# Kernel tuning notes

Measured on AMD Instinct MI355X. Metric: run time of the kernel, lower is better.

## Reference

```python
import jax, jax.numpy as jnp
import numpy as np

N_NODES = 100000
N_EDGES = 1600000
N_FEAT = 128
HID = 64


def setup_inputs() -> dict:
    key = jax.random.key(0)
    ks = jax.random.split(key, 8)
    s = 0.05
    return {
        "x": jax.random.normal(ks[0], (N_NODES, N_FEAT), jnp.float32),
        "edge_index": jax.random.randint(ks[1], (2, N_EDGES), 0, N_NODES, jnp.int64),
        "labels": jax.random.randint(ks[2], (N_NODES, 1), 0, 2, jnp.int32),
        "W1": jax.random.normal(ks[3], (N_FEAT, HID), jnp.float32) * s,
        "b1": jnp.zeros((HID,), jnp.float32),
        "W2": jax.random.normal(ks[4], (HID, HID), jnp.float32) * s,
        "b2": jnp.zeros((HID,), jnp.float32),
        "W3": jax.random.normal(ks[5], (HID, HID), jnp.float32) * s,
        "b3": jnp.zeros((HID,), jnp.float32),
        "lW1": jax.random.normal(ks[6], (HID, 8), jnp.float32) * s,
        "lb1": jnp.zeros((8,), jnp.float32),
        "lW2": jax.random.normal(ks[7], (8, 1), jnp.float32) * s,
        "lb2": jnp.zeros((1,), jnp.float32),
    }


def reference(x, edge_index, labels, W1, b1, W2, b2, W3, b3, lW1, lb1, lW2, lb2):
    n = x.shape[0]
    # PyG GCNConv: add self-loops, symmetric D^{-1/2}(A+I)D^{-1/2} normalization
    loop = jnp.arange(n)
    row = jnp.concatenate([edge_index[0], loop])  # sources
    col = jnp.concatenate([edge_index[1], loop])  # targets (aggregation)
    deg = jax.ops.segment_sum(jnp.ones(col.shape, x.dtype), col, num_segments=n)
    dinv = jax.lax.rsqrt(deg)  # deg >= 1 thanks to self loops
    norm = dinv[row] * dinv[col]  # [E+N]

    def gcn(h, W, b):
        m = (h @ W)[row] * norm[:, None]  # gather + scale per edge
        return jax.ops.segment_sum(m, col, num_segments=n) + b

    h = jax.nn.relu(gcn(x, W1, b1))   # dropout inactive in eval mode
    h = jax.nn.relu(gcn(h, W2, b2))
    h = jax.nn.relu(gcn(h, W3, b3))
    h = jax.nn.relu(h @ lW1 + lb1)
    p = jax.nn.sigmoid(h @ lW2 + lb2)  # [N,1]

    y = labels.astype(x.dtype)
    # generate_weights(labels): class-balance weights (minority class up-weighted)
    pm = jnp.mean(y)
    w = y * (1.0 - pm) + (1.0 - y) * pm
    eps = 1e-7
    pc = jnp.clip(p, eps, 1.0 - eps)
    bce = -(y * jnp.log(pc) + (1.0 - y) * jnp.log(1.0 - pc))
    loss = jnp.mean(w * bce)
    return loss, p
```

## Files before the change

### kernel.cpp

```cpp
#include <hip/hip_runtime.h>
#include <cstdint>
#include <cstddef>

typedef __attribute__((ext_vector_type(8))) short short8;
typedef __attribute__((ext_vector_type(4))) float f32x4;
typedef __attribute__((ext_vector_type(2))) float f32x2;

#define NBLK 512
#define NBLK_SHIFT 9

__device__ inline unsigned short f2bf(float f) {
  union { float f; unsigned int u; } x; x.f = f;
  unsigned int r = x.u + 0x7FFFu + ((x.u >> 16) & 1u);
  return (unsigned short)(r >> 16);
}
__device__ inline float bf2f(unsigned short s) {
  union { unsigned int u; float f; } x; x.u = ((unsigned int)s) << 16;
  return x.f;
}


__global__ __launch_bounds__(256) void hist_kernel(const int* __restrict__ cols,
                                                   int* __restrict__ histG,
                                                   const int* __restrict__ labels,
                                                   float* __restrict__ pmsum,
                                                   const float* __restrict__ W1,
                                                   const float* __restrict__ W2,
                                                   const float* __restrict__ W3,
                                                   unsigned short* __restrict__ Wt1,
                                                   unsigned short* __restrict__ Wt2,
                                                   unsigned short* __restrict__ Wt3,
                                                   int E, int N, int NBUCK) {
  __shared__ int h[512];
  if (blockIdx.x < 3) {
    const float* W; unsigned short* Wt; int K;
    if (blockIdx.x == 0)      { W = W1; Wt = Wt1; K = 128; }
    else if (blockIdx.x == 1) { W = W2; Wt = Wt2; K = 64; }
    else                      { W = W3; Wt = Wt3; K = 64; }
    int total = K * 64;
    for (int i = threadIdx.x; i < total; i += 256) {
      int n = i / K, k = i - n * K;
      Wt[i] = f2bf(W[k * 64 + n]);
    }
  }
  {
    int chunkL = (N + NBLK - 1) / NBLK;
    int ls = blockIdx.x * chunkL;
    int le = min(N, ls + chunkL);
    float v = 0.f;
    for (int i = ls + threadIdx.x; i < le; i += 256) v += (float)labels[i];
#pragma unroll
    for (int o = 32; o > 0; o >>= 1) v += __shfl_down(v, o);
    __shared__ float sl[4];
    if ((threadIdx.x & 63) == 0) sl[threadIdx.x >> 6] = v;
    __syncthreads();
    if (threadIdx.x == 0) {
      float t = sl[0] + sl[1] + sl[2] + sl[3];
      if (t != 0.f) atomicAdd(pmsum, t);
    }
  }
  for (int i = threadIdx.x; i < NBUCK; i += 256) h[i] = 0;
  __syncthreads();
  int chunk = (E + NBLK - 1) / NBLK;
  int s = blockIdx.x * chunk;
  int e = min(E, s + chunk);
  for (int i = s + threadIdx.x; i < e; i += 256) atomicAdd(&h[cols[i] >> 8], 1);
  __syncthreads();
  for (int i = threadIdx.x; i < NBUCK; i += 256)
    histG[blockIdx.x * NBUCK + i] = h[i];
}


__global__ __launch_bounds__(256) void scan_partials_t(const int* __restrict__ histG,
                                                       int* __restrict__ partials,
                                                       int total, int NBUCK) {
  int i = blockIdx.x * 256 + threadIdx.x;
  int v = 0;
  if (i < total) {
    int bucket = i >> NBLK_SHIFT, blk = i & (NBLK - 1);
    v = histG[blk * NBUCK + bucket];
  }
#pragma unroll
  for (int o = 32; o > 0; o >>= 1) v += __shfl_down(v, o);
  __shared__ int s[4];
  if ((threadIdx.x & 63) == 0) s[threadIdx.x >> 6] = v;
  __syncthreads();
  if (threadIdx.x == 0) partials[blockIdx.x] = s[0] + s[1] + s[2] + s[3];
}

__global__ __launch_bounds__(256) void scan_block(int* __restrict__ partials, int nb,
                                                  float* __restrict__ loss) {
  __shared__ int tmp[256];
  __shared__ int carry;
  int tid = threadIdx.x;
  if (tid == 0) { carry = 0; *loss = 0.f; }
  __syncthreads();
  for (int base = 0; base < nb; base += 256) {
    int i = base + tid;
    int v = (i < nb) ? partials[i] : 0;
    tmp[tid] = v;
    __syncthreads();
    int incl = v;
    for (int o = 1; o < 256; o <<= 1) {
      int t = (tid >= o) ? tmp[tid - o] : 0;
      __syncthreads();
      incl += t;
      tmp[tid] = incl;
      __syncthreads();
    }
    int total = tmp[255];
    int c = carry;
    if (i < nb) partials[i] = c + incl - v;
    __syncthreads();
    if (tid == 0) carry = c + total;
    __syncthreads();
  }
}

__global__ __launch_bounds__(256) void scan_final_t(const int* __restrict__ histG,
                                                    const int* __restrict__ partials,
                                                    int* __restrict__ scannedG,
                                                    int total, int NBUCK) {
  __shared__ int tmp[256];
  int tid = threadIdx.x;
  int i = blockIdx.x * 256 + tid;
  int bucket = i >> NBLK_SHIFT, blk = i & (NBLK - 1);
  int v = (i < total) ? histG[blk * NBUCK + bucket] : 0;
  tmp[tid] = v;
  __syncthreads();
  int incl = v;
  for (int o = 1; o < 256; o <<= 1) {
    int t = (tid >= o) ? tmp[tid - o] : 0;
    __syncthreads();
    incl += t;
    tmp[tid] = incl;
    __syncthreads();
  }
  if (i < total) scannedG[blk * NBUCK + bucket] = partials[blockIdx.x] + incl - v;
}


__global__ __launch_bounds__(256) void scatter_kernel(const int* __restrict__ rows,
                                                      const int* __restrict__ cols,
                                                      const int* __restrict__ scannedG,
                                                      unsigned int* __restrict__ packed,
                                                      int E, int NBUCK) {
  __shared__ int cur[512];
  for (int i = threadIdx.x; i < NBUCK; i += 256)
    cur[i] = scannedG[blockIdx.x * NBUCK + i];
  __syncthreads();
  int chunk = (E + NBLK - 1) / NBLK;
  int s = blockIdx.x * chunk;
  int e = min(E, s + chunk);
  for (int i = s + threadIdx.x; i < e; i += 256) {
    int c = cols[i];
    int r = rows[i];
    int pos = atomicAdd(&cur[c >> 8], 1);
    packed[pos] = ((unsigned int)(c & 255) << 24) | (unsigned int)r;
  }
}


__global__ __launch_bounds__(1024) void csr_finalize(const unsigned int* __restrict__ packed,
                                                     const int* __restrict__ scannedG,
                                                     int* __restrict__ sorted_src,
                                                     int* __restrict__ offsets,
                                                     float* __restrict__ dinv,
                                                     int N, int E, int NBUCK) {
  __shared__ int h[256];
  __shared__ int tmp[256];
  __shared__ int cur[256];
  int b = blockIdx.x;
  int tid = threadIdx.x;
  int base = scannedG[b];
  int end = (b + 1 < NBUCK) ? scannedG[b + 1] : E;
  if (tid < 256) h[tid] = 0;
  __syncthreads();
  for (int i = base + tid; i < end; i += 1024)
    atomicAdd(&h[packed[i] >> 24], 1);
  __syncthreads();
  if (tid < 256) {
    int v = h[tid];
    tmp[tid] = v;
  }
  __syncthreads();
  if (tid < 256) {
    int v = h[tid];
    int incl = v;
    for (int o = 1; o < 256; o <<= 1) {
      int t = (tid >= o) ? tmp[tid - o] : 0;
      __syncthreads();
      incl += t;
      tmp[tid] = incl;
      __syncthreads();
    }
    int excl = incl - v;
    int node = b * 256 + tid;
    if (node < N) {
      offsets[node] = base + excl;
      dinv[node] = rsqrtf((float)(v + 1));
    }
    cur[tid] = base + excl;
    if (b == NBUCK - 1 && tid == 0) offsets[N] = E;
  } else {
    for (int o = 1; o < 256; o <<= 1) { __syncthreads(); __syncthreads(); }
  }
  __syncthreads();
  for (int i = base + tid; i < end; i += 1024) {
    unsigned int p = packed[i];
    int pos = atomicAdd(&cur[p >> 24], 1);
    sorted_src[pos] = (int)(p & 0xFFFFFFu);
  }
}


template <int K, bool F32IN>
__global__ __launch_bounds__(256) void mfma_gemm(const void* __restrict__ hv,
                                                 const unsigned short* __restrict__ Wt,
                                                 const float* __restrict__ dinv,
                                                 unsigned char* __restrict__ out, int N) {
  __shared__ unsigned short tile[4][16 * 68];
  int w = threadIdx.x >> 6, lane = threadIdx.x & 63;
  int m = lane & 15, quad = lane >> 4;
  int m0 = blockIdx.x * 64 + w * 16;
  int rowA = m0 + m;
  bool rowOK = rowA < N;
  f32x4 acc[4] = {{0.f,0.f,0.f,0.f},{0.f,0.f,0.f,0.f},{0.f,0.f,0.f,0.f},{0.f,0.f,0.f,0.f}};
#pragma unroll
  for (int kc = 0; kc < K / 32; ++kc) {
    short8 a = {0, 0, 0, 0, 0, 0, 0, 0};
    if (rowOK) {
      if (F32IN) {
        const float* hp = (const float*)hv + (size_t)rowA * K + kc * 32 + quad * 8;
        float4 p0 = ((const float4*)hp)[0];
        float4 p1 = ((const float4*)hp)[1];
        a[0] = (short)f2bf(p0.x); a[1] = (short)f2bf(p0.y);
        a[2] = (short)f2bf(p0.z); a[3] = (short)f2bf(p0.w);
        a[4] = (short)f2bf(p1.x); a[5] = (short)f2bf(p1.y);
        a[6] = (short)f2bf(p1.z); a[7] = (short)f2bf(p1.w);
      } else {
        a = *(const short8*)((const unsigned short*)hv + (size_t)rowA * K + kc * 32 + quad * 8);
      }
    }
#pragma unroll
    for (int t = 0; t < 4; ++t) {
      short8 b = *(const short8*)(Wt + (size_t)(t * 16 + m) * K + kc * 32 + quad * 8);
      acc[t] = __builtin_amdgcn_mfma_f32_16x16x32_bf16(a, b, acc[t], 0, 0, 0);
    }
  }
  unsigned short* tw = tile[w];
#pragma unroll
  for (int r = 0; r < 4; ++r) {
    int row = quad * 4 + r;
    int gr = m0 + row;
    float dv = dinv[gr < N ? gr : 0];
#pragma unroll
    for (int t = 0; t < 4; ++t)
      tw[row * 68 + t * 16 + m] = f2bf(acc[t][r] * dv);
  }
#pragma unroll
  for (int p = 0; p < 4; ++p) {
    int row = p * 4 + (lane >> 4);
    int ch = lane & 15;
    int gr = m0 + row;
    if (gr < N) {
      uint2 v = *(const uint2*)(tw + row * 68 + ch * 4);
      float f0 = bf2f((unsigned short)(v.x & 0xFFFFu));
      float f1 = bf2f((unsigned short)(v.x >> 16));
      float f2 = bf2f((unsigned short)(v.y & 0xFFFFu));
      float f3 = bf2f((unsigned short)(v.y >> 16));
      int pk = 0;
      pk = __builtin_amdgcn_cvt_pk_fp8_f32(f0, f1, pk, false);
      pk = __builtin_amdgcn_cvt_pk_fp8_f32(f2, f3, pk, true);
      *(unsigned int*)(out + (size_t)gr * 64 + ch * 4) = (unsigned int)pk;
    }
  }
}


__global__ __launch_bounds__(256) void aggregate(const unsigned char* __restrict__ A8,
                                                 const int* __restrict__ offsets,
                                                 const int* __restrict__ sorted_src,
                                                 const float* __restrict__ dinv,
                                                 const float* __restrict__ bias,
                                                 unsigned short* __restrict__ out, int N) {
  int c = blockIdx.x * 16 + (threadIdx.x >> 4);
  if (c >= N) return;
  int l = threadIdx.x & 15;
  int qbase = threadIdx.x & 48;
  int g = l >> 3;
  int fi = l & 7;
  int s = offsets[c], e = offsets[c + 1];
  float dc = dinv[c];
  uint2 svr = *(const uint2*)(A8 + (size_t)c * 64 + fi * 8);
  f32x2 a0 = {0.f, 0.f}, a1 = {0.f, 0.f}, a2 = {0.f, 0.f}, a3 = {0.f, 0.f};
  for (int base = s; base < e; base += 16) {
    int idx = base + l;
    int r = (idx < e) ? sorted_src[idx] : 0;
    int cnt = e - base; if (cnt > 16) cnt = 16;
    int rj[8];
#pragma unroll
    for (int t = 0; t < 8; ++t) rj[t] = __shfl(r, qbase + t * 2 + g);
#pragma unroll
    for (int t = 0; t < 8; ++t) {
      if (t * 2 + g < cnt) {
        uint2 v = *(const uint2*)(A8 + ((size_t)(unsigned int)rj[t] << 6) + fi * 8);
        a0 += __builtin_amdgcn_cvt_pk_f32_fp8((int)v.x, false);
        a1 += __builtin_amdgcn_cvt_pk_f32_fp8((int)v.x, true);
        a2 += __builtin_amdgcn_cvt_pk_f32_fp8((int)v.y, false);
        a3 += __builtin_amdgcn_cvt_pk_f32_fp8((int)v.y, true);
      }
    }
  }
  float acc[8] = {a0[0], a0[1], a1[0], a1[1], a2[0], a2[1], a3[0], a3[1]};
#pragma unroll
  for (int q = 0; q < 8; ++q)
    acc[q] += __shfl_xor(acc[q], 8);
  if (g == 0) {
    f32x2 s0 = __builtin_amdgcn_cvt_pk_f32_fp8((int)svr.x, false);
    f32x2 s1 = __builtin_amdgcn_cvt_pk_f32_fp8((int)svr.x, true);
    f32x2 s2 = __builtin_amdgcn_cvt_pk_f32_fp8((int)svr.y, false);
    f32x2 s3 = __builtin_amdgcn_cvt_pk_f32_fp8((int)svr.y, true);
    float sf[8] = {s0[0], s0[1], s1[0], s1[1], s2[0], s2[1], s3[0], s3[1]};
    short8 ov;
#pragma unroll
    for (int q = 0; q < 8; ++q) {
      float v = fmaf(acc[q] + sf[q], dc, bias[fi * 8 + q]);
      ov[q] = (short)f2bf(v > 0.f ? v : 0.f);
    }
    *(short8*)(out + (size_t)c * 64 + fi * 8) = ov;
  }
}


__global__ __launch_bounds__(256) void head_loss_kernel(const unsigned short* __restrict__ h,
                                                        const float* __restrict__ lW1,
                                                        const float* __restrict__ lb1,
                                                        const float* __restrict__ lW2,
                                                        const float* __restrict__ lb2,
                                                        const int* __restrict__ labels,
                                                        const float* __restrict__ pmsum,
                                                        float* __restrict__ p,
                                                        float* __restrict__ loss, int N) {
  int n = blockIdx.x * 256 + threadIdx.x;
  float contrib = 0.f;
  if (n < N) {
    float acc[8];
#pragma unroll
    for (int j = 0; j < 8; ++j) acc[j] = lb1[j];
    const unsigned short* hr = h + (size_t)n * 64;
#pragma unroll
    for (int ch = 0; ch < 8; ++ch) {
      short8 hv8 = ((const short8*)hr)[ch];
#pragma unroll
      for (int q = 0; q < 8; ++q) {
        float v = bf2f((unsigned short)hv8[q]);
        int k = ch * 8 + q;
#pragma unroll
        for (int j = 0; j < 8; ++j) acc[j] = fmaf(v, lW1[k * 8 + j], acc[j]);
      }
    }
    float s = lb2[0];
#pragma unroll
    for (int j = 0; j < 8; ++j) {
      float a = acc[j] > 0.f ? acc[j] : 0.f;
      s = fmaf(a, lW2[j], s);
    }
    float pv = 1.0f / (1.0f + expf(-s));
    p[n] = pv;
    float pm = *pmsum / (float)N;
    float y = (float)labels[n];
    float w = y * (1.f - pm) + (1.f - y) * pm;
    float pc = fminf(fmaxf(pv, 1e-7f), 1.f - 1e-7f);
    float bce = -(y * logf(pc) + (1.f - y) * logf(1.f - pc));
    contrib = w * bce / (float)N;
  }
#pragma unroll
  for (int o = 32; o > 0; o >>= 1) contrib += __shfl_down(contrib, o);
  __shared__ float sh[4];
  int lane = threadIdx.x & 63, w = threadIdx.x >> 6;
  if (lane == 0) sh[w] = contrib;
  __syncthreads();
  if (threadIdx.x == 0) atomicAdd(loss, sh[0] + sh[1] + sh[2] + sh[3]);
}


extern "C" void kernel_launch(void* const* d_in, const int* in_sizes, int n_in,
                              void* d_out, int out_size, void* d_ws, size_t ws_size,
                              hipStream_t stream) {
  const float* x      = (const float*)d_in[0];
  const int*   ei     = (const int*)d_in[1];
  const int*   labels = (const int*)d_in[2];
  const float* W1 = (const float*)d_in[3];
  const float* b1 = (const float*)d_in[4];
  const float* W2 = (const float*)d_in[5];
  const float* b2 = (const float*)d_in[6];
  const float* W3 = (const float*)d_in[7];
  const float* b3 = (const float*)d_in[8];
  const float* lW1 = (const float*)d_in[9];
  const float* lb1 = (const float*)d_in[10];
  const float* lW2 = (const float*)d_in[11];
  const float* lb2 = (const float*)d_in[12];

  int N = in_sizes[2];
  int E = in_sizes[1] / 2;
  const int* rows = ei;
  const int* cols = ei + E;

  int nb = (N + 255) / 256;
  int Npad = (N + 63) & ~63;
  int NBUCK = (N + 255) >> 8;
  int totalH = NBUCK * NBLK;
  int nb2 = (totalH + 255) / 256;

  char* ws = (char*)d_ws;
  unsigned char*  A8  = (unsigned char*)ws;
  unsigned short* H   = (unsigned short*)(ws + (size_t)Npad * 64);
  unsigned short* Wt1 = H + (size_t)Npad * 64;
  unsigned short* Wt2 = Wt1 + 64 * 128;
  unsigned short* Wt3 = Wt2 + 64 * 64;
  float* dinv     = (float*)(Wt3 + 64 * 64);
  int*   offsets  = (int*)(dinv + N);
  int*   histG    = offsets + N + 1;
  int*   scanned  = histG + totalH;
  unsigned int* packed = (unsigned int*)(scanned + totalH);
  int*   sorted   = (int*)(packed + E);
  int*   partials = sorted + E;
  float* pmsum    = (float*)(partials + nb2);

  float* loss = (float*)d_out;
  float* p    = (float*)d_out + 1;

  int gemmBlocks = Npad / 64;
  int aggBlocks  = (N + 15) / 16;

  hipMemsetAsync(pmsum, 0, sizeof(float), stream);
  hist_kernel<<<NBLK, 256, 0, stream>>>(cols, histG, labels, pmsum,
                                        W1, W2, W3, Wt1, Wt2, Wt3, E, N, NBUCK);
  scan_partials_t<<<nb2, 256, 0, stream>>>(histG, partials, totalH, NBUCK);
  scan_block<<<1, 256, 0, stream>>>(partials, nb2, loss);
  scan_final_t<<<nb2, 256, 0, stream>>>(histG, partials, scanned, totalH, NBUCK);
  scatter_kernel<<<NBLK, 256, 0, stream>>>(rows, cols, scanned, packed, E, NBUCK);
  csr_finalize<<<NBUCK, 1024, 0, stream>>>(packed, scanned, sorted, offsets, dinv, N, E, NBUCK);

  mfma_gemm<128, true><<<gemmBlocks, 256, 0, stream>>>(x, Wt1, dinv, A8, N);
  aggregate<<<aggBlocks, 256, 0, stream>>>(A8, offsets, sorted, dinv, b1, H, N);

  mfma_gemm<64, false><<<gemmBlocks, 256, 0, stream>>>(H, Wt2, dinv, A8, N);
  aggregate<<<aggBlocks, 256, 0, stream>>>(A8, offsets, sorted, dinv, b2, H, N);

  mfma_gemm<64, false><<<gemmBlocks, 256, 0, stream>>>(H, Wt3, dinv, A8, N);
  aggregate<<<aggBlocks, 256, 0, stream>>>(A8, offsets, sorted, dinv, b3, H, N);

  head_loss_kernel<<<nb, 256, 0, stream>>>(H, lW1, lb1, lW2, lb2, labels, pmsum, p, loss, N);
}
```

Baseline: 305.2 us.

## Split feature matrices into two 32-column planes and aggregate each plane separately

The GEMM output (fp8) and hidden activations (bf16) are stored as two planes of 32 features each instead of interleaved 64-wide rows. Aggregation runs twice per layer, once per plane, so each pass gathers from a smaller working set (32 bytes per node, about 3.2 MB) that fits better in cache. Each 16-lane group now handles 4 edges in parallel instead of 2. The change also adds nontemporal loads of edge indices and nontemporal output stores. In exchange the edge list and offsets are read twice per layer and there are extra launches.

```diff
diff --git a/kernel.cpp b/kernel.cpp
--- a/kernel.cpp
+++ b/kernel.cpp
@@ -218,7 +218,8 @@
 __global__ __launch_bounds__(256) void mfma_gemm(const void* __restrict__ hv,
                                                  const unsigned short* __restrict__ Wt,
                                                  const float* __restrict__ dinv,
-                                                 unsigned char* __restrict__ out, int N) {
+                                                 unsigned char* __restrict__ out,
+                                                 int N, int Npad) {
   __shared__ unsigned short tile[4][16 * 68];
   int w = threadIdx.x >> 6, lane = threadIdx.x & 63;
   int m = lane & 15, quad = lane >> 4;
@@ -239,7 +240,9 @@
         a[4] = (short)f2bf(p1.x); a[5] = (short)f2bf(p1.y);
         a[6] = (short)f2bf(p1.z); a[7] = (short)f2bf(p1.w);
       } else {
-        a = *(const short8*)((const unsigned short*)hv + (size_t)rowA * K + kc * 32 + quad * 8);
+        const unsigned short* hp = (const unsigned short*)hv +
+            (size_t)kc * ((size_t)Npad * 32) + (size_t)rowA * 32 + quad * 8;
+        a = *(const short8*)hp;
       }
     }
 #pragma unroll
@@ -258,6 +261,7 @@
     for (int t = 0; t < 4; ++t)
       tw[row * 68 + t * 16 + m] = f2bf(acc[t][r] * dv);
   }
+  size_t planeB = (size_t)Npad * 32;
 #pragma unroll
   for (int p = 0; p < 4; ++p) {
     int row = p * 4 + (lane >> 4);
@@ -272,39 +276,42 @@
       int pk = 0;
       pk = __builtin_amdgcn_cvt_pk_fp8_f32(f0, f1, pk, false);
       pk = __builtin_amdgcn_cvt_pk_fp8_f32(f2, f3, pk, true);
-      *(unsigned int*)(out + (size_t)gr * 64 + ch * 4) = (unsigned int)pk;
-    }
-  }
-}
-
-
-__global__ __launch_bounds__(256) void aggregate(const unsigned char* __restrict__ A8,
-                                                 const int* __restrict__ offsets,
-                                                 const int* __restrict__ sorted_src,
-                                                 const float* __restrict__ dinv,
-                                                 const float* __restrict__ bias,
-                                                 unsigned short* __restrict__ out, int N) {
+      *(unsigned int*)(out + (size_t)(ch >> 3) * planeB +
+                       ((size_t)gr << 5) + (size_t)(ch & 7) * 4) = (unsigned int)pk;
+    }
+  }
+}
+
+
+__global__ __launch_bounds__(256) void aggregate_plane(const unsigned char* __restrict__ A8,
+                                                       const int* __restrict__ offsets,
+                                                       const int* __restrict__ sorted_src,
+                                                       const float* __restrict__ dinv,
+                                                       const float* __restrict__ bias,
+                                                       unsigned short* __restrict__ out,
+                                                       int N, int Npad, int plane) {
   int c = blockIdx.x * 16 + (threadIdx.x >> 4);
   if (c >= N) return;
   int l = threadIdx.x & 15;
   int qbase = threadIdx.x & 48;
-  int g = l >> 3;
-  int fi = l & 7;
+  int g = l >> 2;
+  int fi = l & 3;
+  const unsigned char* P = A8 + (size_t)plane * ((size_t)Npad * 32);
   int s = offsets[c], e = offsets[c + 1];
   float dc = dinv[c];
-  uint2 svr = *(const uint2*)(A8 + (size_t)c * 64 + fi * 8);
+  uint2 svr = *(const uint2*)(P + ((size_t)c << 5) + fi * 8);
   f32x2 a0 = {0.f, 0.f}, a1 = {0.f, 0.f}, a2 = {0.f, 0.f}, a3 = {0.f, 0.f};
   for (int base = s; base < e; base += 16) {
     int idx = base + l;
-    int r = (idx < e) ? sorted_src[idx] : 0;
+    int r = (idx < e) ? __builtin_nontemporal_load(sorted_src + idx) : 0;
     int cnt = e - base; if (cnt > 16) cnt = 16;
-    int rj[8];
-#pragma unroll
-    for (int t = 0; t < 8; ++t) rj[t] = __shfl(r, qbase + t * 2 + g);
-#pragma unroll
-    for (int t = 0; t < 8; ++t) {
-      if (t * 2 + g < cnt) {
-        uint2 v = *(const uint2*)(A8 + ((size_t)(unsigned int)rj[t] << 6) + fi * 8);
+    int rj[4];
+#pragma unroll
+    for (int t = 0; t < 4; ++t) rj[t] = __shfl(r, qbase + t * 4 + g);
+#pragma unroll
+    for (int t = 0; t < 4; ++t) {
+      if (t * 4 + g < cnt) {
+        uint2 v = *(const uint2*)(P + ((size_t)(unsigned int)rj[t] << 5) + fi * 8);
         a0 += __builtin_amdgcn_cvt_pk_f32_fp8((int)v.x, false);
         a1 += __builtin_amdgcn_cvt_pk_f32_fp8((int)v.x, true);
         a2 += __builtin_amdgcn_cvt_pk_f32_fp8((int)v.y, false);
@@ -314,21 +321,25 @@
   }
   float acc[8] = {a0[0], a0[1], a1[0], a1[1], a2[0], a2[1], a3[0], a3[1]};
 #pragma unroll
-  for (int q = 0; q < 8; ++q)
+  for (int q = 0; q < 8; ++q) {
+    acc[q] += __shfl_xor(acc[q], 4);
     acc[q] += __shfl_xor(acc[q], 8);
+  }
   if (g == 0) {
     f32x2 s0 = __builtin_amdgcn_cvt_pk_f32_fp8((int)svr.x, false);
     f32x2 s1 = __builtin_amdgcn_cvt_pk_f32_fp8((int)svr.x, true);
     f32x2 s2 = __builtin_amdgcn_cvt_pk_f32_fp8((int)svr.y, false);
     f32x2 s3 = __builtin_amdgcn_cvt_pk_f32_fp8((int)svr.y, true);
     float sf[8] = {s0[0], s0[1], s1[0], s1[1], s2[0], s2[1], s3[0], s3[1]};
+    const float* bp = bias + plane * 32 + fi * 8;
     short8 ov;
 #pragma unroll
     for (int q = 0; q < 8; ++q) {
-      float v = fmaf(acc[q] + sf[q], dc, bias[fi * 8 + q]);
+      float v = fmaf(acc[q] + sf[q], dc, bp[q]);
       ov[q] = (short)f2bf(v > 0.f ? v : 0.f);
     }
-    *(short8*)(out + (size_t)c * 64 + fi * 8) = ov;
+    __builtin_nontemporal_store(ov,
+        (short8*)(out + (size_t)plane * ((size_t)Npad * 32) + (size_t)c * 32 + fi * 8));
   }
 }
 
@@ -341,17 +352,19 @@
                                                         const int* __restrict__ labels,
                                                         const float* __restrict__ pmsum,
                                                         float* __restrict__ p,
-                                                        float* __restrict__ loss, int N) {
+                                                        float* __restrict__ loss,
+                                                        int N, int Npad) {
   int n = blockIdx.x * 256 + threadIdx.x;
   float contrib = 0.f;
   if (n < N) {
     float acc[8];
 #pragma unroll
     for (int j = 0; j < 8; ++j) acc[j] = lb1[j];
-    const unsigned short* hr = h + (size_t)n * 64;
+    size_t planeS = (size_t)Npad * 32;
+    const unsigned short* hr = h + (size_t)n * 32;
 #pragma unroll
     for (int ch = 0; ch < 8; ++ch) {
-      short8 hv8 = ((const short8*)hr)[ch];
+      short8 hv8 = *(const short8*)(hr + (size_t)(ch >> 2) * planeS + (ch & 3) * 8);
 #pragma unroll
       for (int q = 0; q < 8; ++q) {
         float v = bf2f((unsigned short)hv8[q]);
@@ -443,14 +456,17 @@
   scatter_kernel<<<NBLK, 256, 0, stream>>>(rows, cols, scanned, packed, E, NBUCK);
   csr_finalize<<<NBUCK, 1024, 0, stream>>>(packed, scanned, sorted, offsets, dinv, N, E, NBUCK);
 
-  mfma_gemm<128, true><<<gemmBlocks, 256, 0, stream>>>(x, Wt1, dinv, A8, N);
-  aggregate<<<aggBlocks, 256, 0, stream>>>(A8, offsets, sorted, dinv, b1, H, N);
-
-  mfma_gemm<64, false><<<gemmBlocks, 256, 0, stream>>>(H, Wt2, dinv, A8, N);
-  aggregate<<<aggBlocks, 256, 0, stream>>>(A8, offsets, sorted, dinv, b2, H, N);
-
-  mfma_gemm<64, false><<<gemmBlocks, 256, 0, stream>>>(H, Wt3, dinv, A8, N);
-  aggregate<<<aggBlocks, 256, 0, stream>>>(A8, offsets, sorted, dinv, b3, H, N);
-
-  head_loss_kernel<<<nb, 256, 0, stream>>>(H, lW1, lb1, lW2, lb2, labels, pmsum, p, loss, N);
-}
+  mfma_gemm<128, true><<<gemmBlocks, 256, 0, stream>>>(x, Wt1, dinv, A8, N, Npad);
+  aggregate_plane<<<aggBlocks, 256, 0, stream>>>(A8, offsets, sorted, dinv, b1, H, N, Npad, 0);
+  aggregate_plane<<<aggBlocks, 256, 0, stream>>>(A8, offsets, sorted, dinv, b1, H, N, Npad, 1);
+
+  mfma_gemm<64, false><<<gemmBlocks, 256, 0, stream>>>(H, Wt2, dinv, A8, N, Npad);
+  aggregate_plane<<<aggBlocks, 256, 0, stream>>>(A8, offsets, sorted, dinv, b2, H, N, Npad, 0);
+  aggregate_plane<<<aggBlocks, 256, 0, stream>>>(A8, offsets, sorted, dinv, b2, H, N, Npad, 1);
+
+  mfma_gemm<64, false><<<gemmBlocks, 256, 0, stream>>>(H, Wt3, dinv, A8, N, Npad);
+  aggregate_plane<<<aggBlocks, 256, 0, stream>>>(A8, offsets, sorted, dinv, b3, H, N, Npad, 0);
+  aggregate_plane<<<aggBlocks, 256, 0, stream>>>(A8, offsets, sorted, dinv, b3, H, N, Npad, 1);
+
+  head_loss_kernel<<<nb, 256, 0, stream>>>(H, lW1, lb1, lW2, lb2, labels, pmsum, p, loss, N, Npad);
+}
```

After: 341.1 us. 11.8% more time.
